# Performance work log

Hardware: AMD Instinct MI355X
Metric: run time of the kernel (lower is better)

The kernel has to match this reference:

```python
import jax, jax.numpy as jnp
import numpy as np
import math

HEADS = 4
DIM_HEAD = 32
EPS = 1e-5

def _ln_channels(x):
    # LayerNorm over channel axis (axis=1) of NCHW, no affine (eps=1e-5)
    mu = jnp.mean(x, axis=1, keepdims=True)
    var = jnp.mean((x - mu) ** 2, axis=1, keepdims=True)
    return (x - mu) * jax.lax.rsqrt(var + EPS)

def setup_inputs() -> dict:
    key = jax.random.key(0)
    k1, k2, k3, k4 = jax.random.split(key, 4)
    dim, inner = 256, HEADS * DIM_HEAD
    x = jax.random.normal(k1, (16, dim, 64, 64), dtype=jnp.float32)
    Wqkv = jax.random.normal(k2, (3 * inner, dim), dtype=jnp.float32) * (1.0 / math.sqrt(dim))
    Wout = jax.random.normal(k3, (dim, inner), dtype=jnp.float32) * (1.0 / math.sqrt(inner))
    bout = jax.random.normal(k4, (dim,), dtype=jnp.float32) * 0.01
    return {"x": x, "Wqkv": Wqkv, "Wout": Wout, "bout": bout}

def reference(x, Wqkv, Wout, bout):
    B, C, H, W = x.shape
    N = H * W
    inner = HEADS * DIM_HEAD
    # pre-norm (channel-wise LayerNorm via permute in torch)
    normed = _ln_channels(x)
    # 1x1 conv to qkv: [B, 3*inner, H, W]
    qkv = jnp.einsum('oc,bchw->bohw', Wqkv, normed)
    q, k, v = jnp.split(qkv, 3, axis=1)
    # [B, inner, H, W] -> [B, heads, N, dim_head]
    def to_heads(t):
        return t.reshape(B, HEADS, DIM_HEAD, N).transpose(0, 1, 3, 2)
    q, k, v = to_heads(q), to_heads(k), to_heads(v)
    q = jax.nn.softmax(q, axis=-1)          # over dim_head
    k = jax.nn.softmax(k, axis=-2)          # over N
    q = q / math.sqrt(DIM_HEAD)
    v = v / N
    context = jnp.einsum('bhnd,bhne->bhde', k, v)   # [B,h,d,d]
    out = jnp.einsum('bhde,bhnd->bhne', context, q) # [B,h,N,d]
    out = out.transpose(0, 1, 3, 2).reshape(B, inner, H, W)
    out = jnp.einsum('oc,bchw->bohw', Wout, out) + bout[None, :, None, None]
    out = _ln_channels(out)                  # LinearAttention.out_norm
    return out + x                           # residual
```

## Files before the change

### kernel.cpp

```cpp
#include <hip/hip_runtime.h>
#include <hip/hip_bf16.h>
#include <math.h>

#define BATCH 16
#define CH 256
#define NPOS 4096
#define INNER 128
#define HEADS 4
#define DH 32

typedef __hip_bfloat16 bf16;
typedef short bf8v __attribute__((ext_vector_type(8)));
typedef float f32x4 __attribute__((ext_vector_type(4)));

__device__ __forceinline__ float b2f(bf16 v) { return __bfloat162float(v); }
__device__ __forceinline__ float us2f(unsigned short u) {
    unsigned w = ((unsigned)u) << 16; float f; __builtin_memcpy(&f, &w, 4); return f;
}
__device__ __forceinline__ unsigned short f2us(float f) {
    bf16 h = __float2bfloat16(f); unsigned short u; __builtin_memcpy(&u, &h, 2); return u;
}
__device__ __forceinline__ bf16 f2b(float v) { return __float2bfloat16(v); }

__global__ __launch_bounds__(256)
void prep_w_kernel(const float* __restrict__ Wqkv, bf16* __restrict__ wqb,
                   float* __restrict__ wqs) {
    int idx = (blockIdx.x * 256 + threadIdx.x) * 4;
    float4 w = *(const float4*)&Wqkv[idx];
    ushort4 u;
    u.x = f2us(w.x); u.y = f2us(w.y); u.z = f2us(w.z); u.w = f2us(w.w);
    *(ushort4*)&wqb[idx] = u;
    float s4 = us2f(u.x) + us2f(u.y) + us2f(u.z) + us2f(u.w);
    #pragma unroll
    for (int m = 1; m <= 32; m <<= 1) s4 += __shfl_xor(s4, m, 64);
    if ((threadIdx.x & 63) == 0)
        wqs[blockIdx.x * 4 + (threadIdx.x >> 6)] = s4;
}

__global__ __launch_bounds__(256)
void fused_qkv_kernel(const float* __restrict__ x, const bf16* __restrict__ wqb,
                      const float* __restrict__ wqs,
                      bf16* __restrict__ p, float* __restrict__ ctxu) {
    __shared__ char smem[36864];
    __shared__ float stats[640];

    const int b = blockIdx.y, tile = blockIdx.x, n0 = tile * 64;
    const int tid = threadIdx.x;
    const int w = tid >> 6, lane = tid & 63;
    const int lrow = lane & 15, kq = lane >> 4;
    bf16* A = (bf16*)smem;

    {
        const int nq = tid & 15, cp = tid >> 4;
        float s[4] = {0.f,0.f,0.f,0.f}, sq[4] = {0.f,0.f,0.f,0.f};
        #pragma unroll
        for (int i = 0; i < 8; ++i) {
            int c0 = cp * 2 + 32 * i;
            const float* xp = x + ((size_t)b * CH + c0) * NPOS + n0 + nq * 4;
            float4 fa = *(const float4*)xp;
            float4 fb = *(const float4*)(xp + NPOS);
            #pragma unroll
            for (int j = 0; j < 4; ++j) {
                float va = (&fa.x)[j], vb = (&fb.x)[j];
                s[j] += va + vb; sq[j] += va * va + vb * vb;
                *(unsigned*)&A[(nq * 4 + j) * 264 + c0] =
                    (unsigned)f2us(va) | ((unsigned)f2us(vb) << 16);
            }
        }
        #pragma unroll
        for (int j = 0; j < 4; ++j) {
            s[j]  += __shfl_xor(s[j], 16, 64);  sq[j] += __shfl_xor(sq[j], 16, 64);
            s[j]  += __shfl_xor(s[j], 32, 64);  sq[j] += __shfl_xor(sq[j], 32, 64);
            if (lane < 16) {
                stats[(nq * 4 + j) * 8 + w * 2]     = s[j];
                stats[(nq * 4 + j) * 8 + w * 2 + 1] = sq[j];
            }
        }
    }
    __syncthreads();
    if (tid < 64) {
        float s  = stats[tid*8] + stats[tid*8+2] + stats[tid*8+4] + stats[tid*8+6];
        float sq = stats[tid*8+1] + stats[tid*8+3] + stats[tid*8+5] + stats[tid*8+7];
        float m = s * (1.f / 256.f);
        float var = sq * (1.f / 256.f) - m * m;
        stats[512 + tid * 2] = m;
        stats[512 + tid * 2 + 1] = rsqrtf(var + 1e-5f);
    }
    __syncthreads();

    ushort4 ekp[4][2];
    float se0 = 0.f, se1 = 0.f;

    for (int ph = 0; ph < 3; ++ph) {
        const bf16* wp = wqb + (size_t)(ph * 128 + w * 32) * 256;
        const float cs0 = wqs[ph * 128 + w * 32 + lrow];
        const float cs1 = wqs[ph * 128 + w * 32 + 16 + lrow];
        f32x4 acc[4][2];
        #pragma unroll
        for (int i = 0; i < 4; ++i) {
            acc[i][0] = (f32x4){0.f,0.f,0.f,0.f};
            acc[i][1] = (f32x4){0.f,0.f,0.f,0.f};
        }
        #pragma unroll 4
        for (int k0 = 0; k0 < 256; k0 += 32) {
            bf8v af[4], bfr[2];
            #pragma unroll
            for (int t = 0; t < 4; ++t)
                af[t] = *(const bf8v*)&A[(t * 16 + lrow) * 264 + k0 + kq * 8];
            #pragma unroll
            for (int t = 0; t < 2; ++t)
                bfr[t] = *(const bf8v*)&wp[(size_t)(t * 16 + lrow) * 256 + k0 + kq * 8];
            #pragma unroll
            for (int mt = 0; mt < 4; ++mt)
                #pragma unroll
                for (int nt = 0; nt < 2; ++nt)
                    acc[mt][nt] = __builtin_amdgcn_mfma_f32_16x16x32_bf16(
                        af[mt], bfr[nt], acc[mt][nt], 0, 0, 0);
        }

        if (ph == 0) {
            unsigned* pg32 = (unsigned*)p;
            #pragma unroll
            for (int mt = 0; mt < 4; ++mt)
                #pragma unroll
                for (int r = 0; r < 4; ++r) {
                    int row = mt * 16 + kq * 4 + r;
                    float mu = stats[512 + row * 2], rsn = stats[512 + row * 2 + 1];
                    float e0 = __expf(b2f(f2b((acc[mt][0][r] - mu * cs0) * rsn)));
                    float e1 = __expf(b2f(f2b((acc[mt][1][r] - mu * cs1) * rsn)));
                    float s = e0 + e1;
                    s += __shfl_xor(s, 1, 64);  s += __shfl_xor(s, 2, 64);
                    s += __shfl_xor(s, 4, 64);  s += __shfl_xor(s, 8, 64);
                    float rd = 1.f / s;
                    pg32[(size_t)(b * NPOS + n0 + row) * 64 + w * 16 + lrow] =
                        (unsigned)f2us(e0 * rd) | ((unsigned)f2us(e1 * rd) << 16);
                }
        } else if (ph == 1) {
            se0 = 0.f; se1 = 0.f;
            #pragma unroll
            for (int mt = 0; mt < 4; ++mt) {
                ushort4 u0, u1;
                unsigned short q_;
                #pragma unroll
                for (int r = 0; r < 4; ++r) {
                    int row = mt * 16 + kq * 4 + r;
                    float mu = stats[512 + row * 2], rsn = stats[512 + row * 2 + 1];
                    q_ = f2us(__expf(b2f(f2b((acc[mt][0][r] - mu * cs0) * rsn))));
                    se0 += us2f(q_); (&u0.x)[r] = q_;
                    q_ = f2us(__expf(b2f(f2b((acc[mt][1][r] - mu * cs1) * rsn))));
                    se1 += us2f(q_); (&u1.x)[r] = q_;
                }
                ekp[mt][0] = u0; ekp[mt][1] = u1;
            }
            se0 += __shfl_xor(se0, 16, 64); se0 += __shfl_xor(se0, 32, 64);
            se1 += __shfl_xor(se1, 16, 64); se1 += __shfl_xor(se1, 32, 64);
        } else {
            __syncthreads();
            bf16* ekt = (bf16*)(smem + w * 9216);
            bf16* vt  = (bf16*)(smem + w * 9216 + 4608);
            #pragma unroll
            for (int mt = 0; mt < 4; ++mt)
                #pragma unroll
                for (int nt = 0; nt < 2; ++nt) {
                    float csx = nt ? cs1 : cs0;
                    ushort4 vv;
                    #pragma unroll
                    for (int r = 0; r < 4; ++r) {
                        int row = mt * 16 + kq * 4 + r;
                        float mu = stats[512 + row * 2], rsn = stats[512 + row * 2 + 1];
                        (&vv.x)[r] = f2us((acc[mt][nt][r] - mu * csx) * rsn);
                    }
                    int d = nt * 16 + lrow, n = mt * 16 + kq * 4;
                    *(ushort4*)&vt[d * 72 + n]  = vv;
                    *(ushort4*)&ekt[d * 72 + n] = ekp[mt][nt];
                }
            f32x4 cacc[2][2];
            cacc[0][0] = (f32x4){0.f,0.f,0.f,0.f}; cacc[0][1] = cacc[0][0];
            cacc[1][0] = cacc[0][0];               cacc[1][1] = cacc[0][0];
            #pragma unroll
            for (int ks = 0; ks < 2; ++ks) {
                bf8v a2[2], bv2[2];
                a2[0]  = *(const bf8v*)&ekt[lrow * 72 + ks * 32 + kq * 8];
                a2[1]  = *(const bf8v*)&ekt[(16 + lrow) * 72 + ks * 32 + kq * 8];
                bv2[0] = *(const bf8v*)&vt[lrow * 72 + ks * 32 + kq * 8];
                bv2[1] = *(const bf8v*)&vt[(16 + lrow) * 72 + ks * 32 + kq * 8];
                #pragma unroll
                for (int mt2 = 0; mt2 < 2; ++mt2)
                    #pragma unroll
                    for (int nt2 = 0; nt2 < 2; ++nt2)
                        cacc[mt2][nt2] = __builtin_amdgcn_mfma_f32_16x16x32_bf16(
                            a2[mt2], bv2[nt2], cacc[mt2][nt2], 0, 0, 0);
            }
            float* pb = ctxu + ((size_t)(b * HEADS + w)) * 1056;
            #pragma unroll
            for (int mt2 = 0; mt2 < 2; ++mt2)
                #pragma unroll
                for (int nt2 = 0; nt2 < 2; ++nt2)
                    #pragma unroll
                    for (int r = 0; r < 4; ++r) {
                        int d = mt2 * 16 + kq * 4 + r, e = nt2 * 16 + lrow;
                        atomicAdd(&pb[d * 32 + e], cacc[mt2][nt2][r]);
                    }
            if (kq == 0) {
                atomicAdd(&pb[1024 + lrow], se0);
                atomicAdd(&pb[1024 + 16 + lrow], se1);
            }
        }
    }
}

__global__ __launch_bounds__(256)
void ctx_wmod_kernel(const float* __restrict__ ctxu, const float* __restrict__ Wout,
                     bf16* __restrict__ wmod) {
    __shared__ float cs[1056];
    int h = blockIdx.x, b = blockIdx.y, ch = blockIdx.z;
    int tid = threadIdx.x;

    #pragma unroll
    for (int i = 0; i < 2; ++i) {
        int s = i * 256 + tid;
        if (s < 264)
            *(f32x4*)&cs[s * 4] =
                *(const f32x4*)(ctxu + ((size_t)(b * HEADS + h)) * 1056 + s * 4);
    }
    __syncthreads();

    int c = ch * 128 + (tid >> 1);
    int dh = tid & 1;
    const float* wr = Wout + (size_t)c * INNER + h * DH;
    float wv[32];
    #pragma unroll
    for (int i = 0; i < 8; ++i) {
        float4 t = *(const float4*)&wr[i * 4];
        wv[i * 4] = t.x; wv[i * 4 + 1] = t.y; wv[i * 4 + 2] = t.z; wv[i * 4 + 3] = t.w;
    }
    const float SCALE = 4.3158341e-05f;
    unsigned* wm32 = (unsigned*)(wmod + ((size_t)b * CH + c) * INNER + h * DH);
    #pragma unroll
    for (int dd = 0; dd < 8; ++dd) {
        int d1 = dh * 8 + dd, d2 = d1 + 16;
        const float* c1 = &cs[d1 * 32];
        const float* c2 = &cs[d2 * 32];
        float s1 = 0.f, s2 = 0.f;
        #pragma unroll
        for (int e4 = 0; e4 < 8; ++e4) {
            f32x4 t1 = *(const f32x4*)&c1[e4 * 4];
            f32x4 t2 = *(const f32x4*)&c2[e4 * 4];
            #pragma unroll
            for (int j = 0; j < 4; ++j) {
                s1 += wv[e4 * 4 + j] * t1[j];
                s2 += wv[e4 * 4 + j] * t2[j];
            }
        }
        float v1 = s1 * SCALE / cs[1024 + d1];
        float v2 = s2 * SCALE / cs[1024 + d2];
        wm32[d1] = (unsigned)f2us(v1) | ((unsigned)f2us(v2) << 16);
    }
}

__global__ __launch_bounds__(256)
void fused_out_kernel(const bf16* __restrict__ p, const bf16* __restrict__ wmod,
                      const float* __restrict__ bout, const float* __restrict__ x,
                      float* __restrict__ out) {
    __shared__ char lds[37376];
    bf16* Ap = (bf16*)lds;
    float* ct = (float*)lds;
    float* st = (float*)(lds + 34816);

    const int b = blockIdx.y, n0 = blockIdx.x * 64;
    const int tid = threadIdx.x;
    const int w = tid >> 6, lane = tid & 63;
    const int lrow = lane & 15, kq = lane >> 4;

    {
        const uint4* pg = (const uint4*)p;
        unsigned* A32 = (unsigned*)Ap;
        #pragma unroll
        for (int i = 0; i < 4; ++i) {
            int idx = i * 256 + tid;
            int c4 = idx & 15, n = idx >> 4;
            uint4 u = pg[(size_t)(b * NPOS + n0 + n) * 16 + c4];
            *(uint4*)(A32 + n * 68 + c4 * 4) = u;
        }
    }
    __syncthreads();

    f32x4 acc[4][4];
    #pragma unroll
    for (int i = 0; i < 4; ++i)
        #pragma unroll
        for (int j = 0; j < 4; ++j) acc[i][j] = (f32x4){0.f, 0.f, 0.f, 0.f};

    const bf16* wb = wmod + (size_t)b * CH * INNER + (size_t)(w * 64) * INNER;
    #pragma unroll 2
    for (int k0 = 0; k0 < 128; k0 += 32) {
        bf8v af[4], bfr[4];
        #pragma unroll
        for (int t = 0; t < 4; ++t)
            af[t] = *(const bf8v*)&Ap[(t * 16 + lrow) * 136 + k0 + kq * 8];
        #pragma unroll
        for (int t = 0; t < 4; ++t)
            bfr[t] = *(const bf8v*)&wb[(size_t)(t * 16 + lrow) * 128 + k0 + kq * 8];
        #pragma unroll
        for (int mt = 0; mt < 4; ++mt)
            #pragma unroll
            for (int nt = 0; nt < 4; ++nt)
                acc[mt][nt] = __builtin_amdgcn_mfma_f32_16x16x32_bf16(
                    af[mt], bfr[nt], acc[mt][nt], 0, 0, 0);
    }

    #pragma unroll
    for (int nt = 0; nt < 4; ++nt) {
        float bv = bout[w * 64 + nt * 16 + lrow];
        #pragma unroll
        for (int mt = 0; mt < 4; ++mt)
            #pragma unroll
            for (int r = 0; r < 4; ++r) acc[mt][nt][r] += bv;
    }

    #pragma unroll
    for (int mt = 0; mt < 4; ++mt)
        #pragma unroll
        for (int r = 0; r < 4; ++r) {
            float s = 0.f, sq = 0.f;
            #pragma unroll
            for (int nt = 0; nt < 4; ++nt) {
                float v = acc[mt][nt][r];
                s += v; sq += v * v;
            }
            #pragma unroll
            for (int m = 1; m <= 8; m <<= 1) {
                s += __shfl_xor(s, m, 64);
                sq += __shfl_xor(sq, m, 64);
            }
            if (lrow == 0) {
                int row = mt * 16 + kq * 4 + r;
                st[w * 128 + row * 2] = s;
                st[w * 128 + row * 2 + 1] = sq;
            }
        }
    __syncthreads();
    if (tid < 64) {
        float s  = st[tid * 2]       + st[128 + tid * 2]
                 + st[256 + tid * 2] + st[384 + tid * 2];
        float sq = st[tid * 2 + 1]       + st[128 + tid * 2 + 1]
                 + st[256 + tid * 2 + 1] + st[384 + tid * 2 + 1];
        float m = s * (1.f / 256.f);
        float var = sq * (1.f / 256.f) - m * m;
        st[512 + tid * 2] = m;
        st[512 + tid * 2 + 1] = rsqrtf(var + 1e-5f);
    }
    __syncthreads();
    #pragma unroll
    for (int mt = 0; mt < 4; ++mt)
        #pragma unroll
        for (int r = 0; r < 4; ++r) {
            int row = mt * 16 + kq * 4 + r;
            float m = st[512 + row * 2], rs = st[512 + row * 2 + 1];
            #pragma unroll
            for (int nt = 0; nt < 4; ++nt)
                acc[mt][nt][r] = (acc[mt][nt][r] - m) * rs;
        }

    #pragma unroll 1
    for (int pr = 0; pr < 2; ++pr) {
        __syncthreads();
        if ((w >> 1) == pr) {
            #pragma unroll
            for (int mt = 0; mt < 4; ++mt)
                #pragma unroll
                for (int nt = 0; nt < 4; ++nt)
                    #pragma unroll
                    for (int r = 0; r < 4; ++r)
                        ct[((w & 1) * 64 + nt * 16 + lrow) * 68 + mt * 16 + kq * 4 + r]
                            = acc[mt][nt][r];
        }
        __syncthreads();
        #pragma unroll
        for (int i = 0; i < 8; ++i) {
            int idx = i * 256 + tid;
            int n4 = (idx & 15) * 4, cl = idx >> 4;
            size_t gi = ((size_t)b * CH + pr * 128 + cl) * NPOS + n0 + n4;
            f32x4 cv = *(const f32x4*)&ct[cl * 68 + n4];
            f32x4 xv = *(const f32x4*)&x[gi];
            __builtin_nontemporal_store(cv + xv, (f32x4*)&out[gi]);
        }
    }
}

extern "C" void kernel_launch(void* const* d_in, const int* in_sizes, int n_in,
                              void* d_out, int out_size, void* d_ws, size_t ws_size,
                              hipStream_t stream) {
    const float* x    = (const float*)d_in[0];
    const float* Wqkv = (const float*)d_in[1];
    const float* Wout = (const float*)d_in[2];
    const float* bout = (const float*)d_in[3];
    float* out = (float*)d_out;

    char* ws = (char*)d_ws;
    bf16*  p      = (bf16*)ws;
    float* ctxu   = (float*)(ws + 16777216);
    bf16*  wmod   = (bf16*)(ws + 17047552);
    bf16*  wqb    = (bf16*)(ws + 18096128);
    float* wqs    = (float*)(ws + 18292736);

    hipMemsetAsync(ctxu, 0, 270336, stream);
    prep_w_kernel<<<dim3(96), 256, 0, stream>>>(Wqkv, wqb, wqs);
    fused_qkv_kernel<<<dim3(64, BATCH), 256, 0, stream>>>(x, wqb, wqs, p, ctxu);
    ctx_wmod_kernel<<<dim3(HEADS, BATCH, 2), 256, 0, stream>>>(ctxu, Wout, wmod);
    fused_out_kernel<<<dim3(64, BATCH), 256, 0, stream>>>(p, wmod, bout, x, out);
}
```

Measured before the change: 184.7 us.

## Fuse context-to-weight step into QKV kernel via last-block counter; fold memset

Drops the separate ctx_wmod kernel. The last block to finish each batch, detected with an atomic counter and threadfence, now reads the accumulated context and computes the modulated output weights itself. The hipMemsetAsync of the context buffer and counters moves into prep_w_kernel. This removes one launch and one memset, at the cost of a serial tail where 16 single blocks each do the whole batch's weight modulation with less parallelism than before.

```diff
diff --git a/kernel.cpp b/kernel.cpp
--- a/kernel.cpp
+++ b/kernel.cpp
@@ -24,8 +24,9 @@
 
 __global__ __launch_bounds__(256)
 void prep_w_kernel(const float* __restrict__ Wqkv, bf16* __restrict__ wqb,
-                   float* __restrict__ wqs) {
-    int idx = (blockIdx.x * 256 + threadIdx.x) * 4;
+                   float* __restrict__ wqs, uint4* __restrict__ zero_region) {
+    int gid = blockIdx.x * 256 + threadIdx.x;
+    int idx = gid * 4;
     float4 w = *(const float4*)&Wqkv[idx];
     ushort4 u;
     u.x = f2us(w.x); u.y = f2us(w.y); u.z = f2us(w.z); u.w = f2us(w.w);
@@ -35,14 +36,19 @@
     for (int m = 1; m <= 32; m <<= 1) s4 += __shfl_xor(s4, m, 64);
     if ((threadIdx.x & 63) == 0)
         wqs[blockIdx.x * 4 + (threadIdx.x >> 6)] = s4;
+    if (gid < 16900)
+        zero_region[gid] = (uint4){0u, 0u, 0u, 0u};
 }
 
 __global__ __launch_bounds__(256)
 void fused_qkv_kernel(const float* __restrict__ x, const bf16* __restrict__ wqb,
                       const float* __restrict__ wqs,
-                      bf16* __restrict__ p, float* __restrict__ ctxu) {
+                      bf16* __restrict__ p, float* __restrict__ ctxu,
+                      int* __restrict__ cnt, const float* __restrict__ Wout,
+                      bf16* __restrict__ wmod) {
     __shared__ char smem[36864];
     __shared__ float stats[640];
+    __shared__ int lastflag;
 
     const int b = blockIdx.y, tile = blockIdx.x, n0 = tile * 64;
     const int tid = threadIdx.x;
@@ -207,54 +213,47 @@
             }
         }
     }
-}
-
-__global__ __launch_bounds__(256)
-void ctx_wmod_kernel(const float* __restrict__ ctxu, const float* __restrict__ Wout,
-                     bf16* __restrict__ wmod) {
-    __shared__ float cs[1056];
-    int h = blockIdx.x, b = blockIdx.y, ch = blockIdx.z;
-    int tid = threadIdx.x;
-
-    #pragma unroll
-    for (int i = 0; i < 2; ++i) {
-        int s = i * 256 + tid;
-        if (s < 264)
-            *(f32x4*)&cs[s * 4] =
-                *(const f32x4*)(ctxu + ((size_t)(b * HEADS + h)) * 1056 + s * 4);
-    }
-    __syncthreads();
-
-    int c = ch * 128 + (tid >> 1);
-    int dh = tid & 1;
-    const float* wr = Wout + (size_t)c * INNER + h * DH;
-    float wv[32];
-    #pragma unroll
-    for (int i = 0; i < 8; ++i) {
-        float4 t = *(const float4*)&wr[i * 4];
-        wv[i * 4] = t.x; wv[i * 4 + 1] = t.y; wv[i * 4 + 2] = t.z; wv[i * 4 + 3] = t.w;
-    }
-    const float SCALE = 4.3158341e-05f;
-    unsigned* wm32 = (unsigned*)(wmod + ((size_t)b * CH + c) * INNER + h * DH);
-    #pragma unroll
-    for (int dd = 0; dd < 8; ++dd) {
-        int d1 = dh * 8 + dd, d2 = d1 + 16;
-        const float* c1 = &cs[d1 * 32];
-        const float* c2 = &cs[d2 * 32];
-        float s1 = 0.f, s2 = 0.f;
-        #pragma unroll
-        for (int e4 = 0; e4 < 8; ++e4) {
-            f32x4 t1 = *(const f32x4*)&c1[e4 * 4];
-            f32x4 t2 = *(const f32x4*)&c2[e4 * 4];
-            #pragma unroll
-            for (int j = 0; j < 4; ++j) {
-                s1 += wv[e4 * 4 + j] * t1[j];
-                s2 += wv[e4 * 4 + j] * t2[j];
-            }
-        }
-        float v1 = s1 * SCALE / cs[1024 + d1];
-        float v2 = s2 * SCALE / cs[1024 + d2];
-        wm32[d1] = (unsigned)f2us(v1) | ((unsigned)f2us(v2) << 16);
+
+    __threadfence();
+    __syncthreads();
+    if (tid == 0) lastflag = (atomicAdd(&cnt[b], 1) == 63);
+    __syncthreads();
+    if (!lastflag) return;
+    if (tid == 0) cnt[b] = 0;
+
+    float* cs = (float*)smem;
+    for (int i = tid; i < 4224; i += 256)
+        cs[i] = __hip_atomic_load(ctxu + (size_t)b * (HEADS * 1056) + i,
+                                  __ATOMIC_RELAXED, __HIP_MEMORY_SCOPE_AGENT);
+    __syncthreads();
+
+    {
+        const int c = tid;
+        const float SCALE = 4.3158341e-05f;
+        #pragma unroll
+        for (int h = 0; h < HEADS; ++h) {
+            const float* wr = Wout + (size_t)c * INNER + h * DH;
+            const float* chh = cs + h * 1056;
+            unsigned* wm32 = (unsigned*)(wmod + ((size_t)b * CH + c) * INNER + h * DH);
+            for (int d1 = 0; d1 < 16; ++d1) {
+                int d2 = d1 + 16;
+                float s1 = 0.f, s2 = 0.f;
+                #pragma unroll
+                for (int e4 = 0; e4 < 8; ++e4) {
+                    f32x4 wv = *(const f32x4*)&wr[e4 * 4];
+                    f32x4 t1 = *(const f32x4*)&chh[d1 * 32 + e4 * 4];
+                    f32x4 t2 = *(const f32x4*)&chh[d2 * 32 + e4 * 4];
+                    #pragma unroll
+                    for (int j = 0; j < 4; ++j) {
+                        s1 += wv[j] * t1[j];
+                        s2 += wv[j] * t2[j];
+                    }
+                }
+                float v1 = s1 * SCALE / chh[1024 + d1];
+                float v2 = s2 * SCALE / chh[1024 + d2];
+                wm32[d1] = (unsigned)f2us(v1) | ((unsigned)f2us(v2) << 16);
+            }
+        }
     }
 }
 
@@ -400,13 +399,13 @@
     char* ws = (char*)d_ws;
     bf16*  p      = (bf16*)ws;
     float* ctxu   = (float*)(ws + 16777216);
-    bf16*  wmod   = (bf16*)(ws + 17047552);
-    bf16*  wqb    = (bf16*)(ws + 18096128);
-    float* wqs    = (float*)(ws + 18292736);
-
-    hipMemsetAsync(ctxu, 0, 270336, stream);
-    prep_w_kernel<<<dim3(96), 256, 0, stream>>>(Wqkv, wqb, wqs);
-    fused_qkv_kernel<<<dim3(64, BATCH), 256, 0, stream>>>(x, wqb, wqs, p, ctxu);
-    ctx_wmod_kernel<<<dim3(HEADS, BATCH, 2), 256, 0, stream>>>(ctxu, Wout, wmod);
+    int*   cnt    = (int*)(ws + 17047552);
+    bf16*  wmod   = (bf16*)(ws + 17047616);
+    bf16*  wqb    = (bf16*)(ws + 18096192);
+    float* wqs    = (float*)(ws + 18292800);
+
+    prep_w_kernel<<<dim3(96), 256, 0, stream>>>(Wqkv, wqb, wqs, (uint4*)ctxu);
+    fused_qkv_kernel<<<dim3(64, BATCH), 256, 0, stream>>>(x, wqb, wqs, p, ctxu,
+                                                          cnt, Wout, wmod);
     fused_out_kernel<<<dim3(64, BATCH), 256, 0, stream>>>(p, wmod, bout, x, out);
 }
```

Measured after the change: 328.2 us. +77.6%, slower.
